# Kernel tuning notes

Measured on AMD Instinct MI355X. Metric: run time of the kernel, lower is better.

## Reference

```python
import jax, jax.numpy as jnp
import numpy as np
from jax import lax

B, T, C, H, K = 2, 4096, 2048, 16, 4
D = C // H
EPS = 1e-5


def _ln(x, g, b):
    m = x.mean(-1, keepdims=True)
    v = ((x - m) ** 2).mean(-1, keepdims=True)
    return (x - m) / jnp.sqrt(v + EPS) * g + b


def _l2norm(x):
    n = jnp.sqrt(jnp.sum(x * x, axis=-1, keepdims=True))
    return x / jnp.maximum(n, 1e-12)


def setup_inputs() -> dict:
    key = jax.random.key(0)
    ks = jax.random.split(key, 10)
    s = 1.0 / np.sqrt(C)
    x = jax.random.normal(ks[0], (B, T, C), jnp.float32)
    Wq = jax.random.normal(ks[1], (C, C), jnp.float32) * s
    Wk = jax.random.normal(ks[2], (C, C), jnp.float32) * s
    Wv = jax.random.normal(ks[3], (C, C), jnp.float32) * s
    Wo = jax.random.normal(ks[4], (C, C), jnp.float32) * s
    conv_w = jax.random.normal(ks[5], (C, 1, K), jnp.float32) * 0.5  # depthwise (O, I/g, K)
    conv_b = jnp.zeros((C,), jnp.float32)
    Wig = jax.random.normal(ks[6], (C, C), jnp.float32) * 0.02
    big = jnp.full((C,), -2.0, jnp.float32)  # gate_init_bias
    Wog = jax.random.normal(ks[7], (C, C), jnp.float32) * s
    bog = jnp.zeros((C,), jnp.float32)
    Wgam = jax.random.normal(ks[8], (H, C), jnp.float32) * 0.02
    decays = 1.0 - np.exp(np.linspace(np.log(1 - 0.9), np.log(1 - 0.9999), H))
    bgam = jnp.asarray(np.log(decays / (1 - decays)), jnp.float32)
    vn_g = jnp.ones((D,), jnp.float32); vn_b = jnp.zeros((D,), jnp.float32)
    mn_g = jnp.ones((D,), jnp.float32); mn_b = jnp.zeros((D,), jnp.float32)
    gn_g = jnp.ones((C,), jnp.float32); gn_b = jnp.zeros((C,), jnp.float32)
    return dict(x=x, Wq=Wq, Wk=Wk, Wv=Wv, Wo=Wo, conv_w=conv_w, conv_b=conv_b,
                Wig=Wig, big=big, Wog=Wog, bog=bog, Wgam=Wgam, bgam=bgam,
                vn_g=vn_g, vn_b=vn_b, mn_g=mn_g, mn_b=mn_b, gn_g=gn_g, gn_b=gn_b)


def reference(x, Wq, Wk, Wv, Wo, conv_w, conv_b, Wig, big, Wog, bog, Wgam, bgam,
              vn_g, vn_b, mn_g, mn_b, gn_g, gn_b):
    # Causal depthwise conv1d over time
    xt = jnp.transpose(x, (0, 2, 1))                     # [B,C,T]
    xp = jnp.pad(xt, ((0, 0), (0, 0), (K - 1, 0)))
    xc = lax.conv_general_dilated(xp, conv_w, (1,), 'VALID', feature_group_count=C)
    xc = xc + conv_b[None, :, None]
    x_conv = jax.nn.silu(jnp.transpose(xc, (0, 2, 1)))   # [B,T,C]

    q = _l2norm((x @ Wq.T).reshape(B, T, H, D))
    k = _l2norm((x @ Wk.T).reshape(B, T, H, D))
    v = _ln((x @ Wv.T).reshape(B, T, H, D), vn_g, vn_b)
    i_gate = jax.nn.sigmoid(x_conv @ Wig.T + big).reshape(B, T, H, D)
    gamma = jax.nn.sigmoid(x_conv @ Wgam.T + bgam).reshape(B, T, H, 1)

    # Gated linear recurrence: mem_t = gamma_t * mem_{t-1} + i_t * k_t * v_t
    kv = i_gate * k * v
    def combine(c1, c2):
        a1, b1 = c1
        a2, b2 = c2
        return a1 * a2, a2 * b1 + b2
    _, mem = lax.associative_scan(combine, (gamma, kv), axis=1)  # mem: [B,T,H,D]

    mem_out = _ln(mem, mn_g, mn_b)
    out = (mem_out * q).reshape(B * T, H, D)
    # GroupNorm(num_groups=H) over channels
    m = out.mean(-1, keepdims=True)
    var = ((out - m) ** 2).mean(-1, keepdims=True)
    out = (out - m) / jnp.sqrt(var + EPS)
    out = out * gn_g.reshape(H, D) + gn_b.reshape(H, D)
    out = out.reshape(B, T, C)
    out = out * jax.nn.sigmoid(x_conv @ Wog.T + bog)
    return out @ Wo.T
```

## Files before the change

### kernel.cpp

```cpp
#include <hip/hip_runtime.h>
#include <cstdint>
#include <cstddef>

using u16 = unsigned short;
using bf16x8 = __attribute__((ext_vector_type(8))) __bf16;
using f32x4  = __attribute__((ext_vector_type(4))) float;

constexpr int Bb = 2, Tt = 4096, Cc = 2048, Hh = 16, Dd = 128;
constexpr int Mm = Bb * Tt;
constexpr int CHK = 32;
constexpr int NCH = Tt / CHK;
constexpr float EPSf = 1e-5f;

__device__ __forceinline__ u16 f2bf(float f) {
  union { float f; uint32_t u; } v; v.f = f;
  return (u16)((v.u + 0x7fffu + ((v.u >> 16) & 1u)) >> 16);
}
__device__ __forceinline__ float bf2f(u16 h) {
  union { uint32_t u; float f; } v; v.u = ((uint32_t)h) << 16;
  return v.f;
}
__device__ __forceinline__ float sig_(float z) { return 1.f / (1.f + __expf(-z)); }
__device__ __forceinline__ float wred(float v) {
#pragma unroll
  for (int m = 32; m; m >>= 1) v += __shfl_xor(v, m);
  return v;
}
__device__ __forceinline__ float wred32(float v) {
#pragma unroll
  for (int m = 16; m; m >>= 1) v += __shfl_xor(v, m);
  return v;
}
__device__ __forceinline__ void glds16(const u16* g, u16* l) {
  __builtin_amdgcn_global_load_lds(
      (const __attribute__((address_space(1))) unsigned int*)g,
      (__attribute__((address_space(3))) unsigned int*)l, 16, 0, 0);
}
__device__ __forceinline__ void bar_() { asm volatile("s_barrier" ::: "memory"); }

__global__ void la_conv(const float* __restrict__ x, const float* __restrict__ cw,
                        const float* __restrict__ cb, u16* __restrict__ xbf,
                        u16* __restrict__ xconv) {
  int i4 = blockIdx.x * 256 + threadIdx.x;
  int c4 = i4 & (Cc / 4 - 1);
  int bt = i4 >> 9;
  int t = bt & (Tt - 1);
  const float4* x4 = (const float4*)x;
  float4 xv = x4[i4];
  float4 xm1 = t >= 1 ? x4[i4 - Cc / 4] : make_float4(0, 0, 0, 0);
  float4 xm2 = t >= 2 ? x4[i4 - Cc / 2] : make_float4(0, 0, 0, 0);
  float4 xm3 = t >= 3 ? x4[i4 - 3 * Cc / 4] : make_float4(0, 0, 0, 0);
  ushort4 ob; ushort4 oc;
  const float4* cw4 = (const float4*)cw;
  float vv[4]  = {xv.x, xv.y, xv.z, xv.w};
  float v1[4]  = {xm1.x, xm1.y, xm1.z, xm1.w};
  float v2[4]  = {xm2.x, xm2.y, xm2.z, xm2.w};
  float v3[4]  = {xm3.x, xm3.y, xm3.z, xm3.w};
  u16 rb[4], rc[4];
#pragma unroll
  for (int j = 0; j < 4; j++) {
    int c = c4 * 4 + j;
    float4 w = cw4[c];
    float acc = cb[c] + w.w * vv[j] + w.z * v1[j] + w.y * v2[j] + w.x * v3[j];
    rb[j] = f2bf(vv[j]);
    rc[j] = f2bf(acc * sig_(acc));
  }
  ob.x = rb[0]; ob.y = rb[1]; ob.z = rb[2]; ob.w = rb[3];
  oc.x = rc[0]; oc.y = rc[1]; oc.z = rc[2]; oc.w = rc[3];
  ((ushort4*)xbf)[i4] = ob;
  ((ushort4*)xconv)[i4] = oc;
}

__global__ void la_cvt5(const float* w0, const float* w1, const float* w2,
                        const float* w3, const float* w4,
                        u16* o0, u16* o1, u16* o2, u16* o3, u16* o4, int n4each) {
  int i = blockIdx.x * 256 + threadIdx.x;
  int seg = i / n4each;
  int off = i - seg * n4each;
  const float* src = seg == 0 ? w0 : seg == 1 ? w1 : seg == 2 ? w2 : seg == 3 ? w3 : w4;
  u16* dst = seg == 0 ? o0 : seg == 1 ? o1 : seg == 2 ? o2 : seg == 3 ? o3 : o4;
  float4 v = ((const float4*)src)[off];
  ushort4 o;
  o.x = f2bf(v.x); o.y = f2bf(v.y); o.z = f2bf(v.z); o.w = f2bf(v.w);
  ((ushort4*)dst)[off] = o;
}

__global__ __launch_bounds__(256) void la_gamma(
    const u16* __restrict__ xconv, const float* __restrict__ Wg,
    const float* __restrict__ bg, float* __restrict__ gam,
    const float* __restrict__ wo_src, u16* __restrict__ wo_dst) {
  {
    int base = blockIdx.x * 2048;
    for (int i = threadIdx.x; i < 2048; i += 256) {
      float4 v = ((const float4*)wo_src)[base + i];
      ushort4 o;
      o.x = f2bf(v.x); o.y = f2bf(v.y); o.z = f2bf(v.z); o.w = f2bf(v.w);
      ((ushort4*)wo_dst)[base + i] = o;
    }
  }
  __shared__ u16 wlds[Hh * Cc];
  for (int i = threadIdx.x; i < Hh * Cc / 4; i += 256) {
    float4 v = ((const float4*)Wg)[i];
    ushort4 o;
    o.x = f2bf(v.x); o.y = f2bf(v.y); o.z = f2bf(v.z); o.w = f2bf(v.w);
    ((ushort4*)wlds)[i] = o;
  }
  __syncthreads();
  const int wave = threadIdx.x >> 6, lane = threadIdx.x & 63;
  const int row0 = blockIdx.x * 16 + wave * 4;
#pragma unroll
  for (int r = 0; r < 4; r++) {
    const int row = row0 + r;
    const u16* xr = xconv + (size_t)row * Cc + lane * 8;
    bf16x8 xv[4];
#pragma unroll
    for (int it = 0; it < 4; it++) xv[it] = *(const bf16x8*)(xr + it * 512);
#pragma unroll
    for (int h = 0; h < 16; h++) {
      const u16* wr = wlds + h * Cc + lane * 8;
      float acc = 0.f;
#pragma unroll
      for (int it = 0; it < 4; it++) {
        bf16x8 wv = *(const bf16x8*)(wr + it * 512);
#pragma unroll
        for (int e = 0; e < 8; e++) acc += (float)xv[it][e] * (float)wv[e];
      }
      acc = wred(acc);
      if (lane == 0) gam[row * Hh + h] = sig_(acc + bg[h]);
    }
  }
}

__global__ void la_scan1(const u16* pk, const u16* __restrict__ pv,
                         const u16* __restrict__ pig,
                         const float* __restrict__ vng, const float* __restrict__ vnb,
                         const float* __restrict__ bigv,
                         u16* mem, float* gam, float* __restrict__ Ebuf) {
  const int wave = threadIdx.x >> 6, lane = threadIdx.x & 63;
  const int p = blockIdx.x * 4 + wave;
  const int bh = p >> 7, c = p & (NCH - 1);
  const int b = bh >> 4, h = bh & 15;
  const int t0 = c * CHK;
  const size_t rbase = (size_t)b * Tt + t0;
  const size_t base = rbase * Cc + h * Dd + lane * 2;
  float* gp = gam + rbase * Hh + h;
  const int d0 = lane * 2;
  const int c0 = h * Dd + d0;
  const float vg0 = vng[d0], vg1 = vng[d0 + 1];
  const float vb0 = vnb[d0], vb1 = vnb[d0 + 1];
  const float bg0 = bigv[c0], bg1 = bigv[c0 + 1];
  float m0 = 0.f, m1 = 0.f, cg = 1.f;
  for (int tb = 0; tb < CHK; tb += 8) {
    uint32_t uk[8], uv[8], ui[8]; float g[8];
#pragma unroll
    for (int j = 0; j < 8; j++) {
      size_t bb = base + (size_t)(tb + j) * Cc;
      uk[j] = *(const uint32_t*)(pk + bb);
      uv[j] = *(const uint32_t*)(pv + bb);
      ui[j] = *(const uint32_t*)(pig + bb);
      g[j] = gp[(size_t)(tb + j) * Hh];
    }
#pragma unroll
    for (int j = 0; j < 8; j++) {
      float k0 = bf2f((u16)uk[j]), k1 = bf2f((u16)(uk[j] >> 16));
      float v0 = bf2f((u16)uv[j]), v1 = bf2f((u16)(uv[j] >> 16));
      float i0 = bf2f((u16)ui[j]), i1 = bf2f((u16)(ui[j] >> 16));
      float ks = k0 * k0 + k1 * k1;
      float s1 = v0 + v1;
      float s2 = v0 * v0 + v1 * v1;
#pragma unroll
      for (int m = 32; m; m >>= 1) {
        ks += __shfl_xor(ks, m);
        s1 += __shfl_xor(s1, m);
        s2 += __shfl_xor(s2, m);
      }
      float kn = 1.f / fmaxf(sqrtf(ks), 1e-12f);
      float mu = s1 * (1.f / Dd);
      float var = s2 * (1.f / Dd) - mu * mu;
      float rs = rsqrtf(var + EPSf);
      float vh0 = (v0 - mu) * rs * vg0 + vb0;
      float vh1 = (v1 - mu) * rs * vg1 + vb1;
      float kv0 = sig_(i0 + bg0) * (k0 * kn) * vh0;
      float kv1 = sig_(i1 + bg1) * (k1 * kn) * vh1;
      float gg = g[j];
      cg *= gg;
      m0 = fmaf(gg, m0, kv0);
      m1 = fmaf(gg, m1, kv1);
      size_t bb = base + (size_t)(tb + j) * Cc;
      *(uint32_t*)(mem + bb) = (uint32_t)f2bf(m0) | ((uint32_t)f2bf(m1) << 16);
      if (lane == 0) gp[(size_t)(tb + j) * Hh] = cg;
    }
  }
  float2 e; e.x = m0; e.y = m1;
  *(float2*)&Ebuf[(size_t)p * Dd + lane * 2] = e;
}

__global__ void la_scan2(const float* __restrict__ Ebuf, const float* __restrict__ cumg,
                         float* __restrict__ carry) {
  const int bh = blockIdx.x;
  const int b = bh >> 4, h = bh & 15;
  const int lane = threadIdx.x;
  float S0 = 0.f, S1 = 0.f;
  for (int cb = 0; cb < NCH; cb += 8) {
    float2 E[8]; float P[8];
#pragma unroll
    for (int j = 0; j < 8; j++) {
      size_t idx = ((size_t)bh * NCH + cb + j) * Dd + lane * 2;
      E[j] = *(const float2*)&Ebuf[idx];
      P[j] = cumg[((size_t)b * Tt + (cb + j) * CHK + CHK - 1) * Hh + h];
    }
#pragma unroll
    for (int j = 0; j < 8; j++) {
      size_t idx = ((size_t)bh * NCH + cb + j) * Dd + lane * 2;
      float2 s; s.x = S0; s.y = S1;
      *(float2*)&carry[idx] = s;
      S0 = fmaf(P[j], S0, E[j].x);
      S1 = fmaf(P[j], S1, E[j].y);
    }
  }
}

__global__ void la_post(const u16* mem, const u16* qp, const u16* ogp,
                        const float* __restrict__ cumg, const float* __restrict__ carry,
                        const float* __restrict__ mng, const float* __restrict__ mnb,
                        const float* __restrict__ gng, const float* __restrict__ gnb,
                        const float* __restrict__ bog, u16* outb) {
  const int wave = threadIdx.x >> 6, lane = threadIdx.x & 63;
  const int p2 = blockIdx.x * 4 + wave;
  const int row = p2 >> 3, h2 = p2 & 7;
  const int h = h2 * 2 + (lane >> 5);
  const int b = row >> 12, t = row & (Tt - 1), ch = t >> 5;
  const int d0 = (lane & 31) * 4;
  const int c0 = h * Dd + d0;
  const size_t base = (size_t)row * Cc + c0;
  uint2 um = *(const uint2*)(mem + base);
  uint2 uq = *(const uint2*)(qp + base);
  uint2 uo = *(const uint2*)(ogp + base);
  float cg = cumg[(size_t)row * Hh + h];
  float4 cr = *(const float4*)&carry[(((size_t)(b * Hh + h)) * NCH + ch) * Dd + d0];
  float m0 = fmaf(cg, cr.x, bf2f((u16)um.x));
  float m1 = fmaf(cg, cr.y, bf2f((u16)(um.x >> 16)));
  float m2 = fmaf(cg, cr.z, bf2f((u16)um.y));
  float m3 = fmaf(cg, cr.w, bf2f((u16)(um.y >> 16)));
  float q0 = bf2f((u16)uq.x), q1 = bf2f((u16)(uq.x >> 16));
  float q2 = bf2f((u16)uq.y), q3 = bf2f((u16)(uq.y >> 16));
  float g0 = bf2f((u16)uo.x), g1 = bf2f((u16)(uo.x >> 16));
  float g2 = bf2f((u16)uo.y), g3 = bf2f((u16)(uo.y >> 16));
  float qs = wred32(q0*q0 + q1*q1 + q2*q2 + q3*q3);
  float s1 = wred32(m0 + m1 + m2 + m3);
  float s2 = wred32(m0*m0 + m1*m1 + m2*m2 + m3*m3);
  float qn = 1.f / fmaxf(sqrtf(qs), 1e-12f);
  float mu = s1 * (1.f / Dd);
  float var = s2 * (1.f / Dd) - mu * mu;
  float rs = rsqrtf(var + EPSf);
  float4 mg = *(const float4*)&mng[d0];
  float4 mb = *(const float4*)&mnb[d0];
  float o0 = ((m0 - mu) * rs * mg.x + mb.x) * q0 * qn;
  float o1 = ((m1 - mu) * rs * mg.y + mb.y) * q1 * qn;
  float o2 = ((m2 - mu) * rs * mg.z + mb.z) * q2 * qn;
  float o3 = ((m3 - mu) * rs * mg.w + mb.w) * q3 * qn;
  float t1 = wred32(o0 + o1 + o2 + o3);
  float t2 = wred32(o0*o0 + o1*o1 + o2*o2 + o3*o3);
  float mu2 = t1 * (1.f / Dd);
  float var2 = t2 * (1.f / Dd) - mu2 * mu2;
  float rs2 = rsqrtf(var2 + EPSf);
  float4 gg = *(const float4*)&gng[c0];
  float4 gb = *(const float4*)&gnb[c0];
  float4 bo = *(const float4*)&bog[c0];
  float y0 = ((o0 - mu2) * rs2 * gg.x + gb.x) * sig_(g0 + bo.x);
  float y1 = ((o1 - mu2) * rs2 * gg.y + gb.y) * sig_(g1 + bo.y);
  float y2 = ((o2 - mu2) * rs2 * gg.z + gb.z) * sig_(g2 + bo.z);
  float y3 = ((o3 - mu2) * rs2 * gg.w + gb.w) * sig_(g3 + bo.w);
  uint2 out;
  out.x = (uint32_t)f2bf(y0) | ((uint32_t)f2bf(y1) << 16);
  out.y = (uint32_t)f2bf(y2) | ((uint32_t)f2bf(y3) << 16);
  *(uint2*)(outb + base) = out;
}

#define STAGE(t, j) do {                                                        \
    const u16* _s = (((j) == 0 || (j) == 2) ? Ab : Wb)                          \
                    + (((j) == 1 || (j) == 2) ? (size_t)128 * K : (size_t)0)    \
                    + soff + (size_t)(t) * 64;                                  \
    u16* _d = dbase + ((((t) & 1) * 4 + (j)) * 8192);                           \
    glds16(_s, _d);                                                             \
    glds16(_s + 8 * (size_t)K, _d + 512);                                       \
  } while (0)

#define LDFRAG(DST, NFR, SLOT, RBASE) do {                                      \
    _Pragma("unroll")                                                           \
    for (int _i = 0; _i < (NFR); ++_i)                                          \
      _Pragma("unroll")                                                         \
      for (int _ks = 0; _ks < 2; ++_ks)                                         \
        DST[_i][_ks] = *(const bf16x8*)&(SLOT)[((RBASE) + _i * 16) * 64 +       \
                         ((((lane >> 4) + _ks * 4) ^ x7) * 8)];                 \
  } while (0)

#define MM16(QM, QN, AA, BB) do {                                               \
    __builtin_amdgcn_s_setprio(1);                                              \
    _Pragma("unroll")                                                           \
    for (int _mi = 0; _mi < 4; ++_mi)                                           \
      _Pragma("unroll")                                                         \
      for (int _ni = 0; _ni < 2; ++_ni)                                         \
        _Pragma("unroll")                                                       \
        for (int _ks = 0; _ks < 2; ++_ks)                                       \
          acc[QM][QN][_mi][_ni] = __builtin_amdgcn_mfma_f32_16x16x32_bf16(      \
              AA[_mi][_ks], BB[_ni][_ks], acc[QM][QN][_mi][_ni], 0, 0, 0);      \
    __builtin_amdgcn_s_setprio(0);                                              \
  } while (0)

#define MM16_ARD(QM, QN, AA, BB, RSLOT) do {                                    \
    __builtin_amdgcn_s_setprio(1);                                              \
    _Pragma("unroll")                                                           \
    for (int _mi = 0; _mi < 4; ++_mi) {                                         \
      _Pragma("unroll")                                                         \
      for (int _ni = 0; _ni < 2; ++_ni)                                         \
        _Pragma("unroll")                                                       \
        for (int _ks = 0; _ks < 2; ++_ks)                                       \
          acc[QM][QN][_mi][_ni] = __builtin_amdgcn_mfma_f32_16x16x32_bf16(      \
              AA[_mi][_ks], BB[_ni][_ks], acc[QM][QN][_mi][_ni], 0, 0, 0);      \
      _Pragma("unroll")                                                         \
      for (int _ks = 0; _ks < 2; ++_ks)                                         \
        AA[_mi][_ks] = *(const bf16x8*)&(RSLOT)[((ra) + _mi * 16) * 64 +        \
                         ((((lane >> 4) + _ks * 4) ^ x7) * 8)];                 \
    }                                                                           \
    __builtin_amdgcn_s_setprio(0);                                              \
  } while (0)

template <int OUT_BF16>
__global__ __launch_bounds__(512, 2)
void la_gemm(const u16* __restrict__ A0, const u16* __restrict__ A1, int segA2,
             const u16* __restrict__ W0, const u16* __restrict__ W1,
             const u16* __restrict__ W2, const u16* __restrict__ W3,
             const u16* __restrict__ W4,
             void* __restrict__ C0, void* __restrict__ C1, void* __restrict__ C2,
             void* __restrict__ C3, void* __restrict__ C4, int K) {
  __shared__ u16 lds[8 * 8192];
  const int tid  = threadIdx.x;
  const int lane = tid & 63;
  const int wv   = tid >> 6;
  const int wm = wv >> 2;
  const int wn = wv & 3;
  const int fm = lane & 15;
  const int x7 = fm & 7;
  const int seg = blockIdx.x >> 3;
  const int bn = (blockIdx.x & 7) * 256;
  const int bm = blockIdx.y * 256;
  const u16* W = seg == 0 ? W0 : seg == 1 ? W1 : seg == 2 ? W2 : seg == 3 ? W3 : W4;
  void* Co = seg == 0 ? C0 : seg == 1 ? C1 : seg == 2 ? C2 : seg == 3 ? C3 : C4;
  const u16* A = seg < segA2 ? A0 : A1;

  const u16* Ab = A + (size_t)bm * K;
  const u16* Wb = W + (size_t)bn * K;
  const size_t soff = (size_t)(wv * 16 + (lane >> 3)) * K
                      + (size_t)(((lane & 7) ^ (lane >> 3)) * 8);
  u16* const dbase = lds + wv * 1024;
  const int nkt = K >> 6;
  const int ra = wm * 64 + fm;
  const int rb = wn * 32 + fm;

  f32x4 acc[2][2][4][2] = {};
  bf16x8 af[4][2], b0f[2][2], b1f[2][2];

  STAGE(0, 0); STAGE(0, 1); STAGE(0, 2); STAGE(0, 3);
  __builtin_amdgcn_sched_barrier(0);
  STAGE(1, 2); STAGE(1, 1); STAGE(1, 3);
  asm volatile("s_waitcnt vmcnt(6)" ::: "memory");
  bar_();
  LDFRAG(b1f, 2, lds + 1 * 8192, rb);
  LDFRAG(af, 4, lds + 2 * 8192, ra);

  for (int kt = 0; kt < nkt; ++kt) {
    u16* const cur = lds + (kt & 1) * 4 * 8192;
    u16* const nxt = lds + ((kt & 1) ^ 1) * 4 * 8192;

    bar_();
    LDFRAG(b0f, 2, cur + 3 * 8192, rb);
    if (kt + 1 < nkt) STAGE(kt + 1, 0);
    __builtin_amdgcn_sched_barrier(0);
    MM16(1, 1, af, b1f);

    bar_();
    if (kt + 2 < nkt) STAGE(kt + 2, 2);
    __builtin_amdgcn_sched_barrier(0);
    MM16_ARD(1, 0, af, b0f, cur + 0 * 8192);

    bar_();
    if (kt + 2 < nkt) STAGE(kt + 2, 1);
    __builtin_amdgcn_sched_barrier(0);
    MM16(0, 1, af, b1f);
    if (kt < nkt - 2)       asm volatile("s_waitcnt vmcnt(4)" ::: "memory");
    else if (kt == nkt - 2) asm volatile("s_waitcnt vmcnt(0)" ::: "memory");

    bar_();
    if (kt + 1 < nkt) {
      LDFRAG(b1f, 2, nxt + 1 * 8192, rb);
      if (kt + 2 < nkt) STAGE(kt + 2, 3);
      __builtin_amdgcn_sched_barrier(0);
      MM16_ARD(0, 0, af, b0f, nxt + 2 * 8192);
    } else {
      __builtin_amdgcn_sched_barrier(0);
      MM16(0, 0, af, b0f);
    }
  }

  const int cr = (lane >> 4) * 4;
  const int cc = lane & 15;
#pragma unroll
  for (int qm = 0; qm < 2; ++qm)
#pragma unroll
    for (int qn = 0; qn < 2; ++qn)
#pragma unroll
      for (int mi = 0; mi < 4; ++mi)
#pragma unroll
        for (int ni = 0; ni < 2; ++ni)
#pragma unroll
          for (int r = 0; r < 4; ++r) {
            size_t off = (size_t)(bm + qm * 128 + wm * 64 + mi * 16 + cr + r) * Cc
                         + (bn + qn * 128 + wn * 32 + ni * 16 + cc);
            if (OUT_BF16) ((u16*)Co)[off] = f2bf(acc[qm][qn][mi][ni][r]);
            else          ((float*)Co)[off] = acc[qm][qn][mi][ni][r];
          }
}

extern "C" void kernel_launch(void* const* d_in, const int* in_sizes, int n_in,
                              void* d_out, int out_size, void* d_ws, size_t ws_size,
                              hipStream_t stream) {
  (void)in_sizes; (void)n_in; (void)out_size; (void)ws_size;
  const float* x    = (const float*)d_in[0];
  const float* Wq   = (const float*)d_in[1];
  const float* Wk   = (const float*)d_in[2];
  const float* Wv   = (const float*)d_in[3];
  const float* Wo   = (const float*)d_in[4];
  const float* cw   = (const float*)d_in[5];
  const float* cb   = (const float*)d_in[6];
  const float* Wig  = (const float*)d_in[7];
  const float* big  = (const float*)d_in[8];
  const float* Wog  = (const float*)d_in[9];
  const float* bog  = (const float*)d_in[10];
  const float* Wgam = (const float*)d_in[11];
  const float* bgam = (const float*)d_in[12];
  const float* vng  = (const float*)d_in[13];
  const float* vnb  = (const float*)d_in[14];
  const float* mng  = (const float*)d_in[15];
  const float* mnb  = (const float*)d_in[16];
  const float* gng  = (const float*)d_in[17];
  const float* gnb  = (const float*)d_in[18];

  char* ws = (char*)d_ws;
  const size_t NB = (size_t)Mm * Cc * 2;
  u16* xbf   = (u16*)(ws + 0 * NB);
  u16* xconv = (u16*)(ws + 1 * NB);
  u16* preq  = (u16*)(ws + 2 * NB);
  u16* prek  = (u16*)(ws + 3 * NB);
  u16* prev  = (u16*)(ws + 4 * NB);
  u16* preig = (u16*)(ws + 5 * NB);
  u16* wbf   = (u16*)(ws + 6 * NB);
  float* gam = (float*)(ws + 6 * NB + (size_t)Cc * Cc * 2);
  const size_t WE = (size_t)Cc * Cc;
  u16* wk_bf  = preig;
  u16* wv_bf  = preig + WE;
  u16* wig_bf = preig + 2 * WE;
  u16* wog_bf = preig + 3 * WE;
  float* Ebuf  = (float*)preig;
  float* carry = (float*)(preig + 1024 * 1024);
  u16* ogscr = (u16*)d_out;
  u16* igscr = (u16*)((char*)d_out + NB);

  const int WN4 = Cc * Cc / 4;
  dim3 blk(256);
  dim3 gblk(512);

  la_conv<<<Mm * Cc / 4 / 256, blk, 0, stream>>>(x, cw, cb, xbf, xconv);

  la_cvt5<<<5 * WN4 / 256, blk, 0, stream>>>(Wq, Wk, Wv, Wig, Wog,
                                             wbf, wk_bf, wv_bf, wig_bf, wog_bf, WN4);

  la_gemm<1><<<dim3(40, Mm / 256), gblk, 0, stream>>>(
      xbf, xconv, 3, wbf, wk_bf, wv_bf, wig_bf, wog_bf,
      (void*)preq, (void*)prek, (void*)prev, (void*)igscr, (void*)ogscr, Cc);

  la_gamma<<<Mm / 16, blk, 0, stream>>>(xconv, Wgam, bgam, gam, Wo, wbf);

  la_scan1<<<Bb * Hh * NCH / 4, blk, 0, stream>>>(prek, prev, igscr,
                                                  vng, vnb, big, prek, gam, Ebuf);
  la_scan2<<<Bb * Hh, dim3(64), 0, stream>>>(Ebuf, gam, carry);

  la_post<<<Mm * 8 / 4, blk, 0, stream>>>(prek, preq, ogscr, gam, carry,
                                          mng, mnb, gng, gnb, bog, xbf);

  la_gemm<0><<<dim3(8, Mm / 256), gblk, 0, stream>>>(
      xbf, xbf, 5, wbf, wbf, wbf, wbf, wbf,
      d_out, d_out, d_out, d_out, d_out, Cc);
}
```

Baseline: 714.1 us.

## Halve GEMM K-tile to 32 and use half-wave per chunk in scan

The GEMM kernel's K step shrinks from 64 to 32 per stage. That halves LDS use (64KB to 32KB), allows more resident blocks, and changes the swizzle to a 4-way XOR, at the cost of twice as many barriers and loop iterations. Separately, the chunk scan now assigns 32 lanes to each (head, chunk) with 4 channels per lane and 8-byte loads. This cuts shuffle-reduction steps and doubles chunks per block. The GEMMs dominate runtime, so the smaller K tile mainly trades per-iteration overhead against occupancy.

```diff
diff --git a/kernel.cpp b/kernel.cpp
--- a/kernel.cpp
+++ b/kernel.cpp
@@ -136,40 +136,44 @@
                          const float* __restrict__ vng, const float* __restrict__ vnb,
                          const float* __restrict__ bigv,
                          u16* mem, float* gam, float* __restrict__ Ebuf) {
-  const int wave = threadIdx.x >> 6, lane = threadIdx.x & 63;
-  const int p = blockIdx.x * 4 + wave;
+  const int sub  = threadIdx.x >> 5;
+  const int lane = threadIdx.x & 31;
+  const int p = blockIdx.x * 8 + sub;
   const int bh = p >> 7, c = p & (NCH - 1);
   const int b = bh >> 4, h = bh & 15;
   const int t0 = c * CHK;
   const size_t rbase = (size_t)b * Tt + t0;
-  const size_t base = rbase * Cc + h * Dd + lane * 2;
+  const int d0 = lane * 4;
+  const int c0 = h * Dd + d0;
+  const size_t base = rbase * Cc + c0;
   float* gp = gam + rbase * Hh + h;
-  const int d0 = lane * 2;
-  const int c0 = h * Dd + d0;
-  const float vg0 = vng[d0], vg1 = vng[d0 + 1];
-  const float vb0 = vnb[d0], vb1 = vnb[d0 + 1];
-  const float bg0 = bigv[c0], bg1 = bigv[c0 + 1];
-  float m0 = 0.f, m1 = 0.f, cg = 1.f;
+  const float4 vg = *(const float4*)&vng[d0];
+  const float4 vb = *(const float4*)&vnb[d0];
+  const float4 bg = *(const float4*)&bigv[c0];
+  float m0 = 0.f, m1 = 0.f, m2 = 0.f, m3 = 0.f, cg = 1.f;
   for (int tb = 0; tb < CHK; tb += 8) {
-    uint32_t uk[8], uv[8], ui[8]; float g[8];
+    uint2 uk[8], uv[8], ui[8]; float g[8];
 #pragma unroll
     for (int j = 0; j < 8; j++) {
       size_t bb = base + (size_t)(tb + j) * Cc;
-      uk[j] = *(const uint32_t*)(pk + bb);
-      uv[j] = *(const uint32_t*)(pv + bb);
-      ui[j] = *(const uint32_t*)(pig + bb);
+      uk[j] = *(const uint2*)(pk + bb);
+      uv[j] = *(const uint2*)(pv + bb);
+      ui[j] = *(const uint2*)(pig + bb);
       g[j] = gp[(size_t)(tb + j) * Hh];
     }
 #pragma unroll
     for (int j = 0; j < 8; j++) {
-      float k0 = bf2f((u16)uk[j]), k1 = bf2f((u16)(uk[j] >> 16));
-      float v0 = bf2f((u16)uv[j]), v1 = bf2f((u16)(uv[j] >> 16));
-      float i0 = bf2f((u16)ui[j]), i1 = bf2f((u16)(ui[j] >> 16));
-      float ks = k0 * k0 + k1 * k1;
-      float s1 = v0 + v1;
-      float s2 = v0 * v0 + v1 * v1;
-#pragma unroll
-      for (int m = 32; m; m >>= 1) {
+      float k0 = bf2f((u16)uk[j].x), k1 = bf2f((u16)(uk[j].x >> 16));
+      float k2 = bf2f((u16)uk[j].y), k3 = bf2f((u16)(uk[j].y >> 16));
+      float v0 = bf2f((u16)uv[j].x), v1 = bf2f((u16)(uv[j].x >> 16));
+      float v2 = bf2f((u16)uv[j].y), v3 = bf2f((u16)(uv[j].y >> 16));
+      float i0 = bf2f((u16)ui[j].x), i1 = bf2f((u16)(ui[j].x >> 16));
+      float i2 = bf2f((u16)ui[j].y), i3 = bf2f((u16)(ui[j].y >> 16));
+      float ks = k0*k0 + k1*k1 + k2*k2 + k3*k3;
+      float s1 = v0 + v1 + v2 + v3;
+      float s2 = v0*v0 + v1*v1 + v2*v2 + v3*v3;
+#pragma unroll
+      for (int m = 16; m; m >>= 1) {
         ks += __shfl_xor(ks, m);
         s1 += __shfl_xor(s1, m);
         s2 += __shfl_xor(s2, m);
@@ -178,21 +182,30 @@
       float mu = s1 * (1.f / Dd);
       float var = s2 * (1.f / Dd) - mu * mu;
       float rs = rsqrtf(var + EPSf);
-      float vh0 = (v0 - mu) * rs * vg0 + vb0;
-      float vh1 = (v1 - mu) * rs * vg1 + vb1;
-      float kv0 = sig_(i0 + bg0) * (k0 * kn) * vh0;
-      float kv1 = sig_(i1 + bg1) * (k1 * kn) * vh1;
+      float vh0 = (v0 - mu) * rs * vg.x + vb.x;
+      float vh1 = (v1 - mu) * rs * vg.y + vb.y;
+      float vh2 = (v2 - mu) * rs * vg.z + vb.z;
+      float vh3 = (v3 - mu) * rs * vg.w + vb.w;
+      float kv0 = sig_(i0 + bg.x) * (k0 * kn) * vh0;
+      float kv1 = sig_(i1 + bg.y) * (k1 * kn) * vh1;
+      float kv2 = sig_(i2 + bg.z) * (k2 * kn) * vh2;
+      float kv3 = sig_(i3 + bg.w) * (k3 * kn) * vh3;
       float gg = g[j];
       cg *= gg;
       m0 = fmaf(gg, m0, kv0);
       m1 = fmaf(gg, m1, kv1);
+      m2 = fmaf(gg, m2, kv2);
+      m3 = fmaf(gg, m3, kv3);
       size_t bb = base + (size_t)(tb + j) * Cc;
-      *(uint32_t*)(mem + bb) = (uint32_t)f2bf(m0) | ((uint32_t)f2bf(m1) << 16);
+      uint2 om;
+      om.x = (uint32_t)f2bf(m0) | ((uint32_t)f2bf(m1) << 16);
+      om.y = (uint32_t)f2bf(m2) | ((uint32_t)f2bf(m3) << 16);
+      *(uint2*)(mem + bb) = om;
       if (lane == 0) gp[(size_t)(tb + j) * Hh] = cg;
     }
   }
-  float2 e; e.x = m0; e.y = m1;
-  *(float2*)&Ebuf[(size_t)p * Dd + lane * 2] = e;
+  float4 e; e.x = m0; e.y = m1; e.z = m2; e.w = m3;
+  *(float4*)&Ebuf[(size_t)p * Dd + d0] = e;
 }
 
 __global__ void la_scan2(const float* __restrict__ Ebuf, const float* __restrict__ cumg,
@@ -280,48 +293,38 @@
 #define STAGE(t, j) do {                                                        \
     const u16* _s = (((j) == 0 || (j) == 2) ? Ab : Wb)                          \
                     + (((j) == 1 || (j) == 2) ? (size_t)128 * K : (size_t)0)    \
-                    + soff + (size_t)(t) * 64;                                  \
-    u16* _d = dbase + ((((t) & 1) * 4 + (j)) * 8192);                           \
-    glds16(_s, _d);                                                             \
-    glds16(_s + 8 * (size_t)K, _d + 512);                                       \
+                    + soff + (size_t)(t) * 32;                                  \
+    glds16(_s, dbase + ((((t) & 1) * 4 + (j)) * 4096));                         \
   } while (0)
 
 #define LDFRAG(DST, NFR, SLOT, RBASE) do {                                      \
     _Pragma("unroll")                                                           \
     for (int _i = 0; _i < (NFR); ++_i)                                          \
-      _Pragma("unroll")                                                         \
-      for (int _ks = 0; _ks < 2; ++_ks)                                         \
-        DST[_i][_ks] = *(const bf16x8*)&(SLOT)[((RBASE) + _i * 16) * 64 +       \
-                         ((((lane >> 4) + _ks * 4) ^ x7) * 8)];                 \
+      DST[_i] = *(const bf16x8*)&(SLOT)[((RBASE) + _i * 16) * 32 +              \
+                   (((lane >> 4) ^ x3) * 8)];                                   \
   } while (0)
 
-#define MM16(QM, QN, AA, BB) do {                                               \
+#define MM8(QM, QN, AA, BB) do {                                                \
     __builtin_amdgcn_s_setprio(1);                                              \
     _Pragma("unroll")                                                           \
     for (int _mi = 0; _mi < 4; ++_mi)                                           \
       _Pragma("unroll")                                                         \
       for (int _ni = 0; _ni < 2; ++_ni)                                         \
-        _Pragma("unroll")                                                       \
-        for (int _ks = 0; _ks < 2; ++_ks)                                       \
-          acc[QM][QN][_mi][_ni] = __builtin_amdgcn_mfma_f32_16x16x32_bf16(      \
-              AA[_mi][_ks], BB[_ni][_ks], acc[QM][QN][_mi][_ni], 0, 0, 0);      \
+        acc[QM][QN][_mi][_ni] = __builtin_amdgcn_mfma_f32_16x16x32_bf16(        \
+            AA[_mi], BB[_ni], acc[QM][QN][_mi][_ni], 0, 0, 0);                  \
     __builtin_amdgcn_s_setprio(0);                                              \
   } while (0)
 
-#define MM16_ARD(QM, QN, AA, BB, RSLOT) do {                                    \
+#define MM8_ARD(QM, QN, AA, BB, RSLOT) do {                                     \
     __builtin_amdgcn_s_setprio(1);                                              \
     _Pragma("unroll")                                                           \
     for (int _mi = 0; _mi < 4; ++_mi) {                                         \
       _Pragma("unroll")                                                         \
       for (int _ni = 0; _ni < 2; ++_ni)                                         \
-        _Pragma("unroll")                                                       \
-        for (int _ks = 0; _ks < 2; ++_ks)                                       \
-          acc[QM][QN][_mi][_ni] = __builtin_amdgcn_mfma_f32_16x16x32_bf16(      \
-              AA[_mi][_ks], BB[_ni][_ks], acc[QM][QN][_mi][_ni], 0, 0, 0);      \
-      _Pragma("unroll")                                                         \
-      for (int _ks = 0; _ks < 2; ++_ks)                                         \
-        AA[_mi][_ks] = *(const bf16x8*)&(RSLOT)[((ra) + _mi * 16) * 64 +        \
-                         ((((lane >> 4) + _ks * 4) ^ x7) * 8)];                 \
+        acc[QM][QN][_mi][_ni] = __builtin_amdgcn_mfma_f32_16x16x32_bf16(        \
+            AA[_mi], BB[_ni], acc[QM][QN][_mi][_ni], 0, 0, 0);                  \
+      AA[_mi] = *(const bf16x8*)&(RSLOT)[((ra) + _mi * 16) * 32 +               \
+                   (((lane >> 4) ^ x3) * 8)];                                   \
     }                                                                           \
     __builtin_amdgcn_s_setprio(0);                                              \
   } while (0)
@@ -334,14 +337,14 @@
              const u16* __restrict__ W4,
              void* __restrict__ C0, void* __restrict__ C1, void* __restrict__ C2,
              void* __restrict__ C3, void* __restrict__ C4, int K) {
-  __shared__ u16 lds[8 * 8192];
+  __shared__ u16 lds[8 * 4096];
   const int tid  = threadIdx.x;
   const int lane = tid & 63;
   const int wv   = tid >> 6;
   const int wm = wv >> 2;
   const int wn = wv & 3;
   const int fm = lane & 15;
-  const int x7 = fm & 7;
+  const int x3 = (fm >> 1) & 3;
   const int seg = blockIdx.x >> 3;
   const int bn = (blockIdx.x & 7) * 256;
   const int bm = blockIdx.y * 256;
@@ -351,55 +354,55 @@
 
   const u16* Ab = A + (size_t)bm * K;
   const u16* Wb = W + (size_t)bn * K;
-  const size_t soff = (size_t)(wv * 16 + (lane >> 3)) * K
-                      + (size_t)(((lane & 7) ^ (lane >> 3)) * 8);
-  u16* const dbase = lds + wv * 1024;
-  const int nkt = K >> 6;
+  const size_t soff = (size_t)(wv * 16 + (lane >> 2)) * K
+                      + (size_t)((((lane & 3) ^ ((lane >> 3) & 3))) * 8);
+  u16* const dbase = lds + wv * 512;
+  const int nkt = K >> 5;
   const int ra = wm * 64 + fm;
   const int rb = wn * 32 + fm;
 
   f32x4 acc[2][2][4][2] = {};
-  bf16x8 af[4][2], b0f[2][2], b1f[2][2];
+  bf16x8 af[4], b0f[2], b1f[2];
 
   STAGE(0, 0); STAGE(0, 1); STAGE(0, 2); STAGE(0, 3);
   __builtin_amdgcn_sched_barrier(0);
   STAGE(1, 2); STAGE(1, 1); STAGE(1, 3);
-  asm volatile("s_waitcnt vmcnt(6)" ::: "memory");
+  asm volatile("s_waitcnt vmcnt(3)" ::: "memory");
   bar_();
-  LDFRAG(b1f, 2, lds + 1 * 8192, rb);
-  LDFRAG(af, 4, lds + 2 * 8192, ra);
+  LDFRAG(b1f, 2, lds + 1 * 4096, rb);
+  LDFRAG(af, 4, lds + 2 * 4096, ra);
 
   for (int kt = 0; kt < nkt; ++kt) {
-    u16* const cur = lds + (kt & 1) * 4 * 8192;
-    u16* const nxt = lds + ((kt & 1) ^ 1) * 4 * 8192;
+    u16* const cur = lds + (kt & 1) * 4 * 4096;
+    u16* const nxt = lds + ((kt & 1) ^ 1) * 4 * 4096;
 
     bar_();
-    LDFRAG(b0f, 2, cur + 3 * 8192, rb);
+    LDFRAG(b0f, 2, cur + 3 * 4096, rb);
     if (kt + 1 < nkt) STAGE(kt + 1, 0);
     __builtin_amdgcn_sched_barrier(0);
-    MM16(1, 1, af, b1f);
+    MM8(1, 1, af, b1f);
 
     bar_();
     if (kt + 2 < nkt) STAGE(kt + 2, 2);
     __builtin_amdgcn_sched_barrier(0);
-    MM16_ARD(1, 0, af, b0f, cur + 0 * 8192);
+    MM8_ARD(1, 0, af, b0f, cur + 0 * 4096);
 
     bar_();
     if (kt + 2 < nkt) STAGE(kt + 2, 1);
     __builtin_amdgcn_sched_barrier(0);
-    MM16(0, 1, af, b1f);
-    if (kt < nkt - 2)       asm volatile("s_waitcnt vmcnt(4)" ::: "memory");
+    MM8(0, 1, af, b1f);
+    if (kt < nkt - 2)       asm volatile("s_waitcnt vmcnt(2)" ::: "memory");
     else if (kt == nkt - 2) asm volatile("s_waitcnt vmcnt(0)" ::: "memory");
 
     bar_();
     if (kt + 1 < nkt) {
-      LDFRAG(b1f, 2, nxt + 1 * 8192, rb);
+      LDFRAG(b1f, 2, nxt + 1 * 4096, rb);
       if (kt + 2 < nkt) STAGE(kt + 2, 3);
       __builtin_amdgcn_sched_barrier(0);
-      MM16_ARD(0, 0, af, b0f, nxt + 2 * 8192);
+      MM8_ARD(0, 0, af, b0f, nxt + 2 * 4096);
     } else {
       __builtin_amdgcn_sched_barrier(0);
-      MM16(0, 0, af, b0f);
+      MM8(0, 0, af, b0f);
     }
   }
 
@@ -481,7 +484,7 @@
 
   la_gamma<<<Mm / 16, blk, 0, stream>>>(xconv, Wgam, bgam, gam, Wo, wbf);
 
-  la_scan1<<<Bb * Hh * NCH / 4, blk, 0, stream>>>(prek, prev, igscr,
+  la_scan1<<<Bb * Hh * NCH / 8, blk, 0, stream>>>(prek, prev, igscr,
                                                   vng, vnb, big, prek, gam, Ebuf);
   la_scan2<<<Bb * Hh, dim3(64), 0, stream>>>(Ebuf, gam, carry);
 
```

After: 773.8 us. +8.4%, slower.
